# Performance work log

Hardware: AMD Instinct MI355X
Metric: run time of the kernel (lower is better)

The kernel has to match this reference:

```python
import jax, jax.numpy as jnp
import numpy as np

MAX_FEATURES = 5000
EMBED_DIM = 100
H1, H2, NUM_CLASSES = 64, 32, 4
BATCH, SEQ = 1024, 256


def _keras_lstm_scan(x_seq, mask_seq, W, U, b):
    """x_seq: [T,B,E], mask_seq: [T,B] bool. Keras gate order i,f,c,o.
    Masked steps carry (h, c) through unchanged (Keras mask_zero semantics).
    Returns (all hidden states [T,B,H], final hidden [B,H])."""
    B = x_seq.shape[1]
    H = U.shape[0]
    h0 = jnp.zeros((B, H), x_seq.dtype)
    c0 = jnp.zeros((B, H), x_seq.dtype)

    def step(carry, inp):
        h, c = carry
        x, m = inp
        z = x @ W + h @ U + b  # [B, 4H]
        i, f, g, o = jnp.split(z, 4, axis=-1)
        i = jax.nn.sigmoid(i)
        f = jax.nn.sigmoid(f)
        g = jnp.tanh(g)
        o = jax.nn.sigmoid(o)
        c_new = f * c + i * g
        h_new = o * jnp.tanh(c_new)
        m = m[:, None]
        h2 = jnp.where(m, h_new, h)
        c2 = jnp.where(m, c_new, c)
        return (h2, c2), h2

    (hT, _), hs = jax.lax.scan(step, (h0, c0), (x_seq, mask_seq))
    return hs, hT


def setup_inputs() -> dict:
    key = jax.random.key(0)
    ks = jax.random.split(key, 8)
    s = 0.05
    tokens = jax.random.randint(ks[0], (BATCH, SEQ), 0, MAX_FEATURES, dtype=jnp.int32)
    emb = jax.random.normal(ks[1], (MAX_FEATURES, EMBED_DIM), jnp.float32) * s
    W1 = jax.random.normal(ks[2], (EMBED_DIM, 4 * H1), jnp.float32) * s
    U1 = jax.random.normal(ks[3], (H1, 4 * H1), jnp.float32) * s
    b1 = jnp.zeros((4 * H1,), jnp.float32)
    W2 = jax.random.normal(ks[4], (H1, 4 * H2), jnp.float32) * s
    U2 = jax.random.normal(ks[5], (H2, 4 * H2), jnp.float32) * s
    b2 = jnp.zeros((4 * H2,), jnp.float32)
    Wd = jax.random.normal(ks[6], (H2, NUM_CLASSES), jnp.float32) * s
    bd = jnp.zeros((NUM_CLASSES,), jnp.float32)
    return {"tokens": tokens, "emb": emb, "W1": W1, "U1": U1, "b1": b1,
            "W2": W2, "U2": U2, "b2": b2, "Wd": Wd, "bd": bd}


def reference(tokens, emb, W1, U1, b1, W2, U2, b2, Wd, bd):
    mask = (tokens != 0)                       # [B,T] mask_zero=True
    x = emb[tokens]                            # [B,T,E]
    x_t = jnp.transpose(x, (1, 0, 2))          # [T,B,E]
    m_t = jnp.transpose(mask, (1, 0))          # [T,B]
    hs1, _ = _keras_lstm_scan(x_t, m_t, W1, U1, b1)   # [T,B,64]
    _, h2 = _keras_lstm_scan(hs1, m_t, W2, U2, b2)    # [B,32] last valid state
    return jax.nn.sigmoid(h2 @ Wd + bd)        # [B,4]
```

## Files before the change

### kernel.cpp

```cpp
#include <hip/hip_runtime.h>

typedef _Float16 hp2 __attribute__((ext_vector_type(2)));

#define NB    1024
#define TT    256
#define EE    100
#define VOCAB 5000
#define GG1   256
#define GG2   128

__device__ __forceinline__ float fast_sigmoid(float x) {
  return __builtin_amdgcn_rcpf(1.0f + __expf(-x));
}
__device__ __forceinline__ float fast_tanh(float x) {
  return 1.0f - 2.0f * __builtin_amdgcn_rcpf(1.0f + __expf(2.0f * x));
}

__global__ __launch_bounds__(256) void emb_gemm(
    const float* __restrict__ emb, const float* __restrict__ W1,
    const float* __restrict__ b1, float* __restrict__ emb_zi)
{
  __shared__ float sE[8][EE];
  const int j  = threadIdx.x;
  const int v0 = blockIdx.x * 8;
  for (int idx = j; idx < 8 * EE; idx += 256) {
    int r = idx / EE, k = idx % EE;
    sE[r][k] = emb[(size_t)(v0 + r) * EE + k];
  }
  __syncthreads();
  float acc[8];
  const float bb = b1[j];
  #pragma unroll
  for (int r = 0; r < 8; ++r) acc[r] = bb;
  for (int k = 0; k < EE; ++k) {
    float w = W1[k * GG1 + j];
    #pragma unroll
    for (int r = 0; r < 8; ++r) acc[r] = fmaf(sE[r][k], w, acc[r]);
  }
  const int slot = (j & 63) * 4 + (j >> 6);
  #pragma unroll
  for (int r = 0; r < 8; ++r) emb_zi[(size_t)(v0 + r) * GG1 + slot] = acc[r];
}

__global__ __launch_bounds__(64) __attribute__((amdgpu_waves_per_eu(1, 1)))
void lstm_row(
    const int* __restrict__ tokens, const float* __restrict__ emb_zi,
    const float* __restrict__ U1,
    const float* __restrict__ W2, const float* __restrict__ U2, const float* __restrict__ b2,
    const float* __restrict__ Wd, const float* __restrict__ bd,
    float* __restrict__ out)
{
  __shared__ __align__(16) _Float16 sH[96];
  __shared__ int sTok[TT];

  const int u   = threadIdx.x;
  const int row = blockIdx.x;
  const int u2  = u & 31;
  const int s   = u >> 5;

  hp2 wA[128];
  #pragma unroll
  for (int p = 0; p < 32; ++p) {
    #pragma unroll
    for (int g = 0; g < 4; ++g) {
      hp2 w;
      w[0] = (_Float16)U1[(2 * p + 0) * GG1 + g * 64 + u];
      w[1] = (_Float16)U1[(2 * p + 1) * GG1 + g * 64 + u];
      wA[4 * p + g] = w;
    }
  }
  hp2 wB[96];
  #pragma unroll
  for (int p = 0; p < 24; ++p) {
    int k0 = 48 * s + 2 * p;
    const float* r0 = (k0     < 64) ? &W2[(size_t)k0 * GG2]       : &U2[(size_t)(k0 - 64) * GG2];
    const float* r1 = (k0 + 1 < 64) ? &W2[(size_t)(k0 + 1) * GG2] : &U2[(size_t)(k0 + 1 - 64) * GG2];
    #pragma unroll
    for (int g = 0; g < 4; ++g) {
      hp2 w;
      w[0] = (_Float16)r0[g * 32 + u2];
      w[1] = (_Float16)r1[g * 32 + u2];
      wB[4 * p + g] = w;
    }
  }
  const float bi2 = b2[u2], bf2 = b2[32 + u2], bg2 = b2[64 + u2], bo2 = b2[96 + u2];

  ((int4*)sTok)[u] = ((const int4*)(tokens + (size_t)row * TT))[u];
  sH[u] = (_Float16)0.0f;
  if (u < 32) sH[64 + u] = (_Float16)0.0f;
  __syncthreads();

  float c1 = 0.f, h1 = 0.f, c2 = 0.f, h2v = 0.f;
  int tok_cur = sTok[0];
  float4 zx = *(const float4*)&emb_zi[(size_t)tok_cur * GG1 + 4 * u];

  for (int t = 0; t < TT; ++t) {
    const bool m = (tok_cur != 0);
    int tok_next = (t + 1 < TT) ? sTok[t + 1] : 0;

    float a0 = zx.x, a1 = zx.y, a2 = zx.z, a3 = zx.w;
    #pragma unroll
    for (int q = 0; q < 8; ++q) {
      int4 hq = ((const int4*)sH)[q];
      #pragma unroll
      for (int pp = 0; pp < 4; ++pp) {
        hp2 hv = ((const hp2*)&hq)[pp];
        const int p = 4 * q + pp;
        a0 = __builtin_amdgcn_fdot2(hv, wA[4 * p + 0], a0, false);
        a1 = __builtin_amdgcn_fdot2(hv, wA[4 * p + 1], a1, false);
        a2 = __builtin_amdgcn_fdot2(hv, wA[4 * p + 2], a2, false);
        a3 = __builtin_amdgcn_fdot2(hv, wA[4 * p + 3], a3, false);
      }
    }
    float4 zxn = zx;
    if (t + 1 < TT) zxn = *(const float4*)&emb_zi[(size_t)tok_next * GG1 + 4 * u];

    {
      float iv = fast_sigmoid(a0);
      float fv = fast_sigmoid(a1);
      float gv = fast_tanh(a2);
      float ov = fast_sigmoid(a3);
      if (m) { c1 = fv * c1 + iv * gv; h1 = ov * fast_tanh(c1); }
    }
    sH[u] = (_Float16)h1;
    __syncthreads();

    float b0 = 0.f, b1v = 0.f, b2v = 0.f, b3 = 0.f;
    #pragma unroll
    for (int q = 0; q < 6; ++q) {
      int4 hq = ((const int4*)sH)[6 * s + q];
      #pragma unroll
      for (int pp = 0; pp < 4; ++pp) {
        hp2 hv = ((const hp2*)&hq)[pp];
        const int p = 4 * q + pp;
        b0  = __builtin_amdgcn_fdot2(hv, wB[4 * p + 0], b0,  false);
        b1v = __builtin_amdgcn_fdot2(hv, wB[4 * p + 1], b1v, false);
        b2v = __builtin_amdgcn_fdot2(hv, wB[4 * p + 2], b2v, false);
        b3  = __builtin_amdgcn_fdot2(hv, wB[4 * p + 3], b3,  false);
      }
    }
    b0  += __shfl_xor(b0, 32);
    b1v += __shfl_xor(b1v, 32);
    b2v += __shfl_xor(b2v, 32);
    b3  += __shfl_xor(b3, 32);
    {
      float i2 = fast_sigmoid(b0 + bi2);
      float f2 = fast_sigmoid(b1v + bf2);
      float g2 = fast_tanh(b2v + bg2);
      float o2 = fast_sigmoid(b3 + bo2);
      if (m) { c2 = f2 * c2 + i2 * g2; h2v = o2 * fast_tanh(c2); }
    }
    if (s == 0) sH[64 + u2] = (_Float16)h2v;
    __syncthreads();

    tok_cur = tok_next;
    zx = zxn;
  }

  if (u < 4) {
    float a = bd[u];
    #pragma unroll
    for (int k = 0; k < 32; ++k)
      a = fmaf((float)sH[64 + k], Wd[k * 4 + u], a);
    out[(size_t)row * 4 + u] = fast_sigmoid(a);
  }
}

extern "C" void kernel_launch(void* const* d_in, const int* in_sizes, int n_in,
                              void* d_out, int out_size, void* d_ws, size_t ws_size,
                              hipStream_t stream) {
  const int*   tokens = (const int*)d_in[0];
  const float* emb    = (const float*)d_in[1];
  const float* W1     = (const float*)d_in[2];
  const float* U1     = (const float*)d_in[3];
  const float* b1     = (const float*)d_in[4];
  const float* W2     = (const float*)d_in[5];
  const float* U2     = (const float*)d_in[6];
  const float* b2     = (const float*)d_in[7];
  const float* Wd     = (const float*)d_in[8];
  const float* bd     = (const float*)d_in[9];
  float* out    = (float*)d_out;
  float* emb_zi = (float*)d_ws;

  emb_gemm<<<dim3(VOCAB / 8), dim3(256), 0, stream>>>(emb, W1, b1, emb_zi);
  lstm_row<<<dim3(NB), dim3(64), 0, stream>>>(
      tokens, emb_zi, U1, W2, U2, b2, Wd, bd, out);
}
```

Measured before the change: 241.6 us.

## Skew LSTM layers by one step with double-buffered hidden state

Layer 2 at step t now runs in the same loop iteration as layer 1 at step t+1. Both read one shared-memory buffer and write the other, which cuts the per-step barriers from two to one and lets the two layers' dot-product chains interleave for more ILP. The embedding projection prefetch moves two steps ahead, and the first layer-1 step is peeled before the loop. The cost is extra prologue code, a second small LDS buffer and a fiddlier mask and token bookkeeping, with the final layer-2 state read from buffer 0.

```diff
diff --git a/kernel.cpp b/kernel.cpp
--- a/kernel.cpp
+++ b/kernel.cpp
@@ -50,7 +50,7 @@
     const float* __restrict__ Wd, const float* __restrict__ bd,
     float* __restrict__ out)
 {
-  __shared__ __align__(16) _Float16 sH[96];
+  __shared__ __align__(16) _Float16 sHB[2][96];
   __shared__ int sTok[TT];
 
   const int u   = threadIdx.x;
@@ -86,22 +86,43 @@
   const float bi2 = b2[u2], bf2 = b2[32 + u2], bg2 = b2[64 + u2], bo2 = b2[96 + u2];
 
   ((int4*)sTok)[u] = ((const int4*)(tokens + (size_t)row * TT))[u];
-  sH[u] = (_Float16)0.0f;
-  if (u < 32) sH[64 + u] = (_Float16)0.0f;
+  sHB[0][u] = (_Float16)0.0f;
+  sHB[1][u] = (_Float16)0.0f;
+  if (u < 32) { sHB[0][64 + u] = (_Float16)0.0f; sHB[1][64 + u] = (_Float16)0.0f; }
   __syncthreads();
 
-  float c1 = 0.f, h1 = 0.f, c2 = 0.f, h2v = 0.f;
-  int tok_cur = sTok[0];
-  float4 zx = *(const float4*)&emb_zi[(size_t)tok_cur * GG1 + 4 * u];
+  float c1 = 0.f, h1r = 0.f, c2 = 0.f, h2r = 0.f;
+
+  int tok_b = sTok[0];
+  {
+    float4 zx0 = *(const float4*)&emb_zi[(size_t)tok_b * GG1 + 4 * u];
+    if (tok_b != 0) {
+      float iv = fast_sigmoid(zx0.x), fv = fast_sigmoid(zx0.y);
+      float gv = fast_tanh(zx0.z),    ov = fast_sigmoid(zx0.w);
+      (void)fv;
+      c1 = iv * gv; h1r = ov * fast_tanh(c1);
+    }
+    sHB[0][u] = (_Float16)h1r;
+  }
+  int   tok_a = sTok[1];
+  float4 zxa = *(const float4*)&emb_zi[(size_t)tok_a * GG1 + 4 * u];
+  __syncthreads();
 
   for (int t = 0; t < TT; ++t) {
-    const bool m = (tok_cur != 0);
-    int tok_next = (t + 1 < TT) ? sTok[t + 1] : 0;
-
-    float a0 = zx.x, a1 = zx.y, a2 = zx.z, a3 = zx.w;
+    const _Float16* rb = sHB[t & 1];
+    _Float16*       wb = (_Float16*)sHB[(t & 1) ^ 1];
+
+    int tok_n = 0;
+    float4 zxn = zxa;
+    if (t + 2 < TT) {
+      tok_n = sTok[t + 2];
+      zxn = *(const float4*)&emb_zi[(size_t)tok_n * GG1 + 4 * u];
+    }
+
+    float a0 = zxa.x, a1 = zxa.y, a2 = zxa.z, a3 = zxa.w;
     #pragma unroll
     for (int q = 0; q < 8; ++q) {
-      int4 hq = ((const int4*)sH)[q];
+      int4 hq = ((const int4*)rb)[q];
       #pragma unroll
       for (int pp = 0; pp < 4; ++pp) {
         hp2 hv = ((const hp2*)&hq)[pp];
@@ -112,23 +133,12 @@
         a3 = __builtin_amdgcn_fdot2(hv, wA[4 * p + 3], a3, false);
       }
     }
-    float4 zxn = zx;
-    if (t + 1 < TT) zxn = *(const float4*)&emb_zi[(size_t)tok_next * GG1 + 4 * u];
-
-    {
-      float iv = fast_sigmoid(a0);
-      float fv = fast_sigmoid(a1);
-      float gv = fast_tanh(a2);
-      float ov = fast_sigmoid(a3);
-      if (m) { c1 = fv * c1 + iv * gv; h1 = ov * fast_tanh(c1); }
-    }
-    sH[u] = (_Float16)h1;
-    __syncthreads();
 
     float b0 = 0.f, b1v = 0.f, b2v = 0.f, b3 = 0.f;
+    const int4* hbp = (const int4*)(rb + 48 * s);
     #pragma unroll
     for (int q = 0; q < 6; ++q) {
-      int4 hq = ((const int4*)sH)[6 * s + q];
+      int4 hq = hbp[q];
       #pragma unroll
       for (int pp = 0; pp < 4; ++pp) {
         hp2 hv = ((const hp2*)&hq)[pp];
@@ -139,29 +149,40 @@
         b3  = __builtin_amdgcn_fdot2(hv, wB[4 * p + 3], b3,  false);
       }
     }
+
     b0  += __shfl_xor(b0, 32);
     b1v += __shfl_xor(b1v, 32);
     b2v += __shfl_xor(b2v, 32);
     b3  += __shfl_xor(b3, 32);
     {
+      const bool mb = (tok_b != 0);
       float i2 = fast_sigmoid(b0 + bi2);
       float f2 = fast_sigmoid(b1v + bf2);
       float g2 = fast_tanh(b2v + bg2);
       float o2 = fast_sigmoid(b3 + bo2);
-      if (m) { c2 = f2 * c2 + i2 * g2; h2v = o2 * fast_tanh(c2); }
-    }
-    if (s == 0) sH[64 + u2] = (_Float16)h2v;
+      if (mb) { c2 = f2 * c2 + i2 * g2; h2r = o2 * fast_tanh(c2); }
+    }
+    if (s == 0) wb[64 + u2] = (_Float16)h2r;
+
+    {
+      const bool ma = (tok_a != 0);
+      float iv = fast_sigmoid(a0);
+      float fv = fast_sigmoid(a1);
+      float gv = fast_tanh(a2);
+      float ov = fast_sigmoid(a3);
+      if (ma) { c1 = fv * c1 + iv * gv; h1r = ov * fast_tanh(c1); }
+    }
+    wb[u] = (_Float16)h1r;
     __syncthreads();
 
-    tok_cur = tok_next;
-    zx = zxn;
+    tok_b = tok_a; tok_a = tok_n; zxa = zxn;
   }
 
   if (u < 4) {
     float a = bd[u];
     #pragma unroll
     for (int k = 0; k < 32; ++k)
-      a = fmaf((float)sH[64 + k], Wd[k * 4 + u], a);
+      a = fmaf((float)sHB[0][64 + k], Wd[k * 4 + u], a);
     out[(size_t)row * 4 + u] = fast_sigmoid(a);
   }
 }
```

Result: slower. 251.8 us (+4.2%).

## Process two batch rows per wavefront to interleave independent LSTM recurrences

Applied to the files above, without the earlier changes.

Each 64-thread block now advances two sequences at once, sharing the register-resident U1/W2/U2 weights and issuing two independent dot-product chains per step. The aim is to hide the latency of the serial recurrence and barriers with a second independent stream of work, and to halve the per-block weight loading. In exchange the grid is halved to 512 blocks, which on a 256-CU part may leave fewer waves per CU, and each thread needs more registers.

```diff
diff --git a/kernel.cpp b/kernel.cpp
--- a/kernel.cpp
+++ b/kernel.cpp
@@ -43,18 +43,18 @@
 }
 
 __global__ __launch_bounds__(64) __attribute__((amdgpu_waves_per_eu(1, 1)))
-void lstm_row(
+void lstm_row2(
     const int* __restrict__ tokens, const float* __restrict__ emb_zi,
     const float* __restrict__ U1,
     const float* __restrict__ W2, const float* __restrict__ U2, const float* __restrict__ b2,
     const float* __restrict__ Wd, const float* __restrict__ bd,
     float* __restrict__ out)
 {
-  __shared__ __align__(16) _Float16 sH[96];
-  __shared__ int sTok[TT];
+  __shared__ __align__(16) _Float16 sH[2][96];
+  __shared__ int sTok[2][TT];
 
   const int u   = threadIdx.x;
-  const int row = blockIdx.x;
+  const int b   = blockIdx.x;
   const int u2  = u & 31;
   const int s   = u >> 5;
 
@@ -85,84 +85,114 @@
   }
   const float bi2 = b2[u2], bf2 = b2[32 + u2], bg2 = b2[64 + u2], bo2 = b2[96 + u2];
 
-  ((int4*)sTok)[u] = ((const int4*)(tokens + (size_t)row * TT))[u];
-  sH[u] = (_Float16)0.0f;
-  if (u < 32) sH[64 + u] = (_Float16)0.0f;
+  ((int4*)sTok[0])[u] = ((const int4*)(tokens + (size_t)(2 * b + 0) * TT))[u];
+  ((int4*)sTok[1])[u] = ((const int4*)(tokens + (size_t)(2 * b + 1) * TT))[u];
+  sH[0][u] = (_Float16)0.0f;
+  sH[1][u] = (_Float16)0.0f;
+  if (u < 32) { sH[0][64 + u] = (_Float16)0.0f; sH[1][64 + u] = (_Float16)0.0f; }
   __syncthreads();
 
-  float c1 = 0.f, h1 = 0.f, c2 = 0.f, h2v = 0.f;
-  int tok_cur = sTok[0];
-  float4 zx = *(const float4*)&emb_zi[(size_t)tok_cur * GG1 + 4 * u];
+  float c1A = 0.f, h1A = 0.f, c2A = 0.f, h2A = 0.f;
+  float c1B = 0.f, h1B = 0.f, c2B = 0.f, h2B = 0.f;
+  int tokA = sTok[0][0];
+  int tokB = sTok[1][0];
+  float4 zxA = *(const float4*)&emb_zi[(size_t)tokA * GG1 + 4 * u];
+  float4 zxB = *(const float4*)&emb_zi[(size_t)tokB * GG1 + 4 * u];
 
   for (int t = 0; t < TT; ++t) {
-    const bool m = (tok_cur != 0);
-    int tok_next = (t + 1 < TT) ? sTok[t + 1] : 0;
-
-    float a0 = zx.x, a1 = zx.y, a2 = zx.z, a3 = zx.w;
+    const bool mA = (tokA != 0), mB = (tokB != 0);
+    int tokAn = 0, tokBn = 0;
+    if (t + 1 < TT) { tokAn = sTok[0][t + 1]; tokBn = sTok[1][t + 1]; }
+
+    float aA0 = zxA.x, aA1 = zxA.y, aA2 = zxA.z, aA3 = zxA.w;
+    float aB0 = zxB.x, aB1 = zxB.y, aB2 = zxB.z, aB3 = zxB.w;
     #pragma unroll
     for (int q = 0; q < 8; ++q) {
-      int4 hq = ((const int4*)sH)[q];
+      int4 hqA = ((const int4*)sH[0])[q];
+      int4 hqB = ((const int4*)sH[1])[q];
       #pragma unroll
       for (int pp = 0; pp < 4; ++pp) {
-        hp2 hv = ((const hp2*)&hq)[pp];
         const int p = 4 * q + pp;
-        a0 = __builtin_amdgcn_fdot2(hv, wA[4 * p + 0], a0, false);
-        a1 = __builtin_amdgcn_fdot2(hv, wA[4 * p + 1], a1, false);
-        a2 = __builtin_amdgcn_fdot2(hv, wA[4 * p + 2], a2, false);
-        a3 = __builtin_amdgcn_fdot2(hv, wA[4 * p + 3], a3, false);
+        hp2 hvA = ((const hp2*)&hqA)[pp];
+        hp2 hvB = ((const hp2*)&hqB)[pp];
+        aA0 = __builtin_amdgcn_fdot2(hvA, wA[4 * p + 0], aA0, false);
+        aA1 = __builtin_amdgcn_fdot2(hvA, wA[4 * p + 1], aA1, false);
+        aA2 = __builtin_amdgcn_fdot2(hvA, wA[4 * p + 2], aA2, false);
+        aA3 = __builtin_amdgcn_fdot2(hvA, wA[4 * p + 3], aA3, false);
+        aB0 = __builtin_amdgcn_fdot2(hvB, wA[4 * p + 0], aB0, false);
+        aB1 = __builtin_amdgcn_fdot2(hvB, wA[4 * p + 1], aB1, false);
+        aB2 = __builtin_amdgcn_fdot2(hvB, wA[4 * p + 2], aB2, false);
+        aB3 = __builtin_amdgcn_fdot2(hvB, wA[4 * p + 3], aB3, false);
       }
     }
-    float4 zxn = zx;
-    if (t + 1 < TT) zxn = *(const float4*)&emb_zi[(size_t)tok_next * GG1 + 4 * u];
-
+    float4 zxAn = zxA, zxBn = zxB;
+    if (t + 1 < TT) {
+      zxAn = *(const float4*)&emb_zi[(size_t)tokAn * GG1 + 4 * u];
+      zxBn = *(const float4*)&emb_zi[(size_t)tokBn * GG1 + 4 * u];
+    }
     {
-      float iv = fast_sigmoid(a0);
-      float fv = fast_sigmoid(a1);
-      float gv = fast_tanh(a2);
-      float ov = fast_sigmoid(a3);
-      if (m) { c1 = fv * c1 + iv * gv; h1 = ov * fast_tanh(c1); }
-    }
-    sH[u] = (_Float16)h1;
+      float iv = fast_sigmoid(aA0), fv = fast_sigmoid(aA1);
+      float gv = fast_tanh(aA2),    ov = fast_sigmoid(aA3);
+      if (mA) { c1A = fv * c1A + iv * gv; h1A = ov * fast_tanh(c1A); }
+      float iw = fast_sigmoid(aB0), fw = fast_sigmoid(aB1);
+      float gw = fast_tanh(aB2),    ow = fast_sigmoid(aB3);
+      if (mB) { c1B = fw * c1B + iw * gw; h1B = ow * fast_tanh(c1B); }
+    }
+    sH[0][u] = (_Float16)h1A;
+    sH[1][u] = (_Float16)h1B;
     __syncthreads();
 
-    float b0 = 0.f, b1v = 0.f, b2v = 0.f, b3 = 0.f;
+    float bA0 = 0.f, bA1 = 0.f, bA2 = 0.f, bA3 = 0.f;
+    float bB0 = 0.f, bB1 = 0.f, bB2 = 0.f, bB3 = 0.f;
+    const int4* hpA = (const int4*)(&sH[0][48 * s]);
+    const int4* hpB = (const int4*)(&sH[1][48 * s]);
     #pragma unroll
     for (int q = 0; q < 6; ++q) {
-      int4 hq = ((const int4*)sH)[6 * s + q];
+      int4 hqA = hpA[q];
+      int4 hqB = hpB[q];
       #pragma unroll
       for (int pp = 0; pp < 4; ++pp) {
-        hp2 hv = ((const hp2*)&hq)[pp];
         const int p = 4 * q + pp;
-        b0  = __builtin_amdgcn_fdot2(hv, wB[4 * p + 0], b0,  false);
-        b1v = __builtin_amdgcn_fdot2(hv, wB[4 * p + 1], b1v, false);
-        b2v = __builtin_amdgcn_fdot2(hv, wB[4 * p + 2], b2v, false);
-        b3  = __builtin_amdgcn_fdot2(hv, wB[4 * p + 3], b3,  false);
+        hp2 hvA = ((const hp2*)&hqA)[pp];
+        hp2 hvB = ((const hp2*)&hqB)[pp];
+        bA0 = __builtin_amdgcn_fdot2(hvA, wB[4 * p + 0], bA0, false);
+        bA1 = __builtin_amdgcn_fdot2(hvA, wB[4 * p + 1], bA1, false);
+        bA2 = __builtin_amdgcn_fdot2(hvA, wB[4 * p + 2], bA2, false);
+        bA3 = __builtin_amdgcn_fdot2(hvA, wB[4 * p + 3], bA3, false);
+        bB0 = __builtin_amdgcn_fdot2(hvB, wB[4 * p + 0], bB0, false);
+        bB1 = __builtin_amdgcn_fdot2(hvB, wB[4 * p + 1], bB1, false);
+        bB2 = __builtin_amdgcn_fdot2(hvB, wB[4 * p + 2], bB2, false);
+        bB3 = __builtin_amdgcn_fdot2(hvB, wB[4 * p + 3], bB3, false);
       }
     }
-    b0  += __shfl_xor(b0, 32);
-    b1v += __shfl_xor(b1v, 32);
-    b2v += __shfl_xor(b2v, 32);
-    b3  += __shfl_xor(b3, 32);
+    bA0 += __shfl_xor(bA0, 32); bA1 += __shfl_xor(bA1, 32);
+    bA2 += __shfl_xor(bA2, 32); bA3 += __shfl_xor(bA3, 32);
+    bB0 += __shfl_xor(bB0, 32); bB1 += __shfl_xor(bB1, 32);
+    bB2 += __shfl_xor(bB2, 32); bB3 += __shfl_xor(bB3, 32);
     {
-      float i2 = fast_sigmoid(b0 + bi2);
-      float f2 = fast_sigmoid(b1v + bf2);
-      float g2 = fast_tanh(b2v + bg2);
-      float o2 = fast_sigmoid(b3 + bo2);
-      if (m) { c2 = f2 * c2 + i2 * g2; h2v = o2 * fast_tanh(c2); }
-    }
-    if (s == 0) sH[64 + u2] = (_Float16)h2v;
+      float i2 = fast_sigmoid(bA0 + bi2), f2 = fast_sigmoid(bA1 + bf2);
+      float g2 = fast_tanh(bA2 + bg2),    o2 = fast_sigmoid(bA3 + bo2);
+      if (mA) { c2A = f2 * c2A + i2 * g2; h2A = o2 * fast_tanh(c2A); }
+      float i3 = fast_sigmoid(bB0 + bi2), f3 = fast_sigmoid(bB1 + bf2);
+      float g3 = fast_tanh(bB2 + bg2),    o3 = fast_sigmoid(bB3 + bo2);
+      if (mB) { c2B = f3 * c2B + i3 * g3; h2B = o3 * fast_tanh(c2B); }
+    }
+    if (s == 0) {
+      sH[0][64 + u2] = (_Float16)h2A;
+      sH[1][64 + u2] = (_Float16)h2B;
+    }
     __syncthreads();
 
-    tok_cur = tok_next;
-    zx = zxn;
-  }
-
-  if (u < 4) {
-    float a = bd[u];
+    tokA = tokAn; tokB = tokBn; zxA = zxAn; zxB = zxBn;
+  }
+
+  if (u < 8) {
+    int r = u >> 2, o = u & 3;
+    float a = bd[o];
     #pragma unroll
     for (int k = 0; k < 32; ++k)
-      a = fmaf((float)sH[64 + k], Wd[k * 4 + u], a);
-    out[(size_t)row * 4 + u] = fast_sigmoid(a);
+      a = fmaf((float)sH[r][64 + k], Wd[k * 4 + o], a);
+    out[(size_t)(2 * b + r) * 4 + o] = fast_sigmoid(a);
   }
 }
 
@@ -183,6 +213,6 @@
   float* emb_zi = (float*)d_ws;
 
   emb_gemm<<<dim3(VOCAB / 8), dim3(256), 0, stream>>>(emb, W1, b1, emb_zi);
-  lstm_row<<<dim3(NB), dim3(64), 0, stream>>>(
+  lstm_row2<<<dim3(NB / 2), dim3(64), 0, stream>>>(
       tokens, emb_zi, U1, W2, U2, b2, Wd, bd, out);
 }
```

Result: slower. 487.4 us (+101.7%).

## Batch 16 rows per block with MFMA recurrences and layer-pipelined waves

Applied to the files above, without the earlier changes.

Replaces the one-row-per-64-thread-block LSTM with blocks that each process 16 batch rows and compute both recurrent matmuls with 16x16x16 fp16 MFMA instructions. Four waves compute layer 1 and two waves compute layer 2. Layer 2 runs one timestep behind layer 1 through a double-buffered shared fragment buffer, so each timestep needs a single barrier. This targets the serial dot-product latency and the low occupancy of the old per-row scheme. The costs are only 64 blocks for the whole batch, a larger per-step critical path through a 6-wave barrier, and fragment-layout indexing that is easy to get wrong.

```diff
diff --git a/kernel.cpp b/kernel.cpp
--- a/kernel.cpp
+++ b/kernel.cpp
@@ -1,6 +1,7 @@
 #include <hip/hip_runtime.h>
 
-typedef _Float16 hp2 __attribute__((ext_vector_type(2)));
+typedef _Float16 h4 __attribute__((ext_vector_type(4)));
+typedef float    f4v __attribute__((ext_vector_type(4)));
 
 #define NB    1024
 #define TT    256
@@ -8,6 +9,8 @@
 #define VOCAB 5000
 #define GG1   256
 #define GG2   128
+#define RPB   16
+#define NTHR  384
 
 __device__ __forceinline__ float fast_sigmoid(float x) {
   return __builtin_amdgcn_rcpf(1.0f + __expf(-x));
@@ -42,127 +45,179 @@
   for (int r = 0; r < 8; ++r) emb_zi[(size_t)(v0 + r) * GG1 + slot] = acc[r];
 }
 
-__global__ __launch_bounds__(64) __attribute__((amdgpu_waves_per_eu(1, 1)))
-void lstm_row(
+__global__ __launch_bounds__(NTHR, 2) void lstm_mfma(
     const int* __restrict__ tokens, const float* __restrict__ emb_zi,
     const float* __restrict__ U1,
     const float* __restrict__ W2, const float* __restrict__ U2, const float* __restrict__ b2,
     const float* __restrict__ Wd, const float* __restrict__ bd,
     float* __restrict__ out)
 {
-  __shared__ __align__(16) _Float16 sH[96];
-  __shared__ int sTok[TT];
-
-  const int u   = threadIdx.x;
-  const int row = blockIdx.x;
-  const int u2  = u & 31;
-  const int s   = u >> 5;
-
-  hp2 wA[128];
-  #pragma unroll
-  for (int p = 0; p < 32; ++p) {
-    #pragma unroll
-    for (int g = 0; g < 4; ++g) {
-      hp2 w;
-      w[0] = (_Float16)U1[(2 * p + 0) * GG1 + g * 64 + u];
-      w[1] = (_Float16)U1[(2 * p + 1) * GG1 + g * 64 + u];
-      wA[4 * p + g] = w;
+  __shared__ __align__(16) _Float16 fbuf[2][6][256];
+  __shared__ __align__(16) int sTokT[TT][16];
+  __shared__ float hfin[RPB][32];
+
+  const int tid  = threadIdx.x;
+  const int w    = tid >> 6;
+  const int l    = tid & 63;
+  const int lr   = l & 15;
+  const int lg   = l >> 4;
+  const int row0 = blockIdx.x * RPB;
+
+  h4 wB[4][6];
+  float bias2[4] = {0.f, 0.f, 0.f, 0.f};
+  if (w < 4) {
+    #pragma unroll
+    for (int gi = 0; gi < 4; ++gi) {
+      #pragma unroll
+      for (int c = 0; c < 4; ++c) {
+        h4 v;
+        #pragma unroll
+        for (int jj = 0; jj < 4; ++jj) {
+          int k = 16 * c + lg * 4 + jj;
+          v[jj] = (_Float16)U1[k * GG1 + 64 * gi + 16 * w + lr];
+        }
+        wB[gi][c] = v;
+      }
     }
-  }
-  hp2 wB[96];
-  #pragma unroll
-  for (int p = 0; p < 24; ++p) {
-    int k0 = 48 * s + 2 * p;
-    const float* r0 = (k0     < 64) ? &W2[(size_t)k0 * GG2]       : &U2[(size_t)(k0 - 64) * GG2];
-    const float* r1 = (k0 + 1 < 64) ? &W2[(size_t)(k0 + 1) * GG2] : &U2[(size_t)(k0 + 1 - 64) * GG2];
-    #pragma unroll
-    for (int g = 0; g < 4; ++g) {
-      hp2 w;
-      w[0] = (_Float16)r0[g * 32 + u2];
-      w[1] = (_Float16)r1[g * 32 + u2];
-      wB[4 * p + g] = w;
+  } else {
+    const int w2 = w - 4;
+    #pragma unroll
+    for (int gi = 0; gi < 4; ++gi) {
+      #pragma unroll
+      for (int c = 0; c < 6; ++c) {
+        h4 v;
+        #pragma unroll
+        for (int jj = 0; jj < 4; ++jj) {
+          int k  = 16 * c + lg * 4 + jj;
+          int j2 = 32 * gi + 16 * w2 + lr;
+          float x = (k < 64) ? W2[k * GG2 + j2] : U2[(k - 64) * GG2 + j2];
+          v[jj] = (_Float16)x;
+        }
+        wB[gi][c] = v;
+      }
+      bias2[gi] = b2[32 * gi + 16 * w2 + lr];
     }
   }
-  const float bi2 = b2[u2], bf2 = b2[32 + u2], bg2 = b2[64 + u2], bo2 = b2[96 + u2];
-
-  ((int4*)sTok)[u] = ((const int4*)(tokens + (size_t)row * TT))[u];
-  sH[u] = (_Float16)0.0f;
-  if (u < 32) sH[64 + u] = (_Float16)0.0f;
+
+  for (int idx = tid; idx < RPB * TT; idx += NTHR) {
+    int m = idx >> 8, t = idx & 255;
+    sTokT[t][m] = tokens[(size_t)(row0 + m) * TT + t];
+  }
+  for (int idx = tid; idx < 2 * 6 * 256; idx += NTHR)
+    ((_Float16*)fbuf)[idx] = (_Float16)0.0f;
   __syncthreads();
 
-  float c1 = 0.f, h1 = 0.f, c2 = 0.f, h2v = 0.f;
-  int tok_cur = sTok[0];
-  float4 zx = *(const float4*)&emb_zi[(size_t)tok_cur * GG1 + 4 * u];
-
-  for (int t = 0; t < TT; ++t) {
-    const bool m = (tok_cur != 0);
-    int tok_next = (t + 1 < TT) ? sTok[t + 1] : 0;
-
-    float a0 = zx.x, a1 = zx.y, a2 = zx.z, a3 = zx.w;
-    #pragma unroll
-    for (int q = 0; q < 8; ++q) {
-      int4 hq = ((const int4*)sH)[q];
-      #pragma unroll
-      for (int pp = 0; pp < 4; ++pp) {
-        hp2 hv = ((const hp2*)&hq)[pp];
-        const int p = 4 * q + pp;
-        a0 = __builtin_amdgcn_fdot2(hv, wA[4 * p + 0], a0, false);
-        a1 = __builtin_amdgcn_fdot2(hv, wA[4 * p + 1], a1, false);
-        a2 = __builtin_amdgcn_fdot2(hv, wA[4 * p + 2], a2, false);
-        a3 = __builtin_amdgcn_fdot2(hv, wA[4 * p + 3], a3, false);
+  float c1v[4] = {0.f,0.f,0.f,0.f}, h1v[4] = {0.f,0.f,0.f,0.f};
+  float c2v[4] = {0.f,0.f,0.f,0.f}, h2v[4] = {0.f,0.f,0.f,0.f};
+
+  f4v zx[4];
+  if (w < 4) {
+    int4 tk0 = *(const int4*)&sTokT[0][lg * 4];
+    const int uu = 16 * w + lr;
+    zx[0] = *(const f4v*)&emb_zi[(size_t)tk0.x * GG1 + uu * 4];
+    zx[1] = *(const f4v*)&emb_zi[(size_t)tk0.y * GG1 + uu * 4];
+    zx[2] = *(const f4v*)&emb_zi[(size_t)tk0.z * GG1 + uu * 4];
+    zx[3] = *(const f4v*)&emb_zi[(size_t)tk0.w * GG1 + uu * 4];
+  }
+
+  for (int t = 0; t <= TT; ++t) {
+    const int p = t & 1;
+    if (w < 4) {
+      if (t < TT) {
+        h4 a0 = *(const h4*)&fbuf[p][0][l * 4];
+        h4 a1 = *(const h4*)&fbuf[p][1][l * 4];
+        h4 a2 = *(const h4*)&fbuf[p][2][l * 4];
+        h4 a3 = *(const h4*)&fbuf[p][3][l * 4];
+        f4v ac[4];
+        #pragma unroll
+        for (int gi = 0; gi < 4; ++gi) {
+          f4v s;
+          s[0] = zx[0][gi]; s[1] = zx[1][gi]; s[2] = zx[2][gi]; s[3] = zx[3][gi];
+          s = __builtin_amdgcn_mfma_f32_16x16x16f16(a0, wB[gi][0], s, 0, 0, 0);
+          s = __builtin_amdgcn_mfma_f32_16x16x16f16(a1, wB[gi][1], s, 0, 0, 0);
+          s = __builtin_amdgcn_mfma_f32_16x16x16f16(a2, wB[gi][2], s, 0, 0, 0);
+          s = __builtin_amdgcn_mfma_f32_16x16x16f16(a3, wB[gi][3], s, 0, 0, 0);
+          ac[gi] = s;
+        }
+        f4v zn[4];
+        #pragma unroll
+        for (int i = 0; i < 4; ++i) zn[i] = zx[i];
+        if (t + 1 < TT) {
+          int4 tkn = *(const int4*)&sTokT[t + 1][lg * 4];
+          const int uu = 16 * w + lr;
+          zn[0] = *(const f4v*)&emb_zi[(size_t)tkn.x * GG1 + uu * 4];
+          zn[1] = *(const f4v*)&emb_zi[(size_t)tkn.y * GG1 + uu * 4];
+          zn[2] = *(const f4v*)&emb_zi[(size_t)tkn.z * GG1 + uu * 4];
+          zn[3] = *(const f4v*)&emb_zi[(size_t)tkn.w * GG1 + uu * 4];
+        }
+        int4 tk = *(const int4*)&sTokT[t][lg * 4];
+        int tka[4] = {tk.x, tk.y, tk.z, tk.w};
+        #pragma unroll
+        for (int i = 0; i < 4; ++i) {
+          float iv = fast_sigmoid(ac[0][i]);
+          float fv = fast_sigmoid(ac[1][i]);
+          float gv = fast_tanh(ac[2][i]);
+          float ov = fast_sigmoid(ac[3][i]);
+          float cn = fv * c1v[i] + iv * gv;
+          if (tka[i] != 0) { c1v[i] = cn; h1v[i] = ov * fast_tanh(cn); }
+          fbuf[p ^ 1][w][(lg * 4 + i + 16 * (lr >> 2)) * 4 + (lr & 3)] = (_Float16)h1v[i];
+        }
+        #pragma unroll
+        for (int i = 0; i < 4; ++i) zx[i] = zn[i];
+      }
+    } else {
+      if (t >= 1) {
+        const int tt = t - 1;
+        const int w2 = w - 4;
+        h4 a0 = *(const h4*)&fbuf[p][0][l * 4];
+        h4 a1 = *(const h4*)&fbuf[p][1][l * 4];
+        h4 a2 = *(const h4*)&fbuf[p][2][l * 4];
+        h4 a3 = *(const h4*)&fbuf[p][3][l * 4];
+        h4 a4 = *(const h4*)&fbuf[p][4][l * 4];
+        h4 a5 = *(const h4*)&fbuf[p][5][l * 4];
+        f4v ac[4];
+        #pragma unroll
+        for (int gi = 0; gi < 4; ++gi) {
+          f4v s;
+          s[0] = bias2[gi]; s[1] = bias2[gi]; s[2] = bias2[gi]; s[3] = bias2[gi];
+          s = __builtin_amdgcn_mfma_f32_16x16x16f16(a0, wB[gi][0], s, 0, 0, 0);
+          s = __builtin_amdgcn_mfma_f32_16x16x16f16(a1, wB[gi][1], s, 0, 0, 0);
+          s = __builtin_amdgcn_mfma_f32_16x16x16f16(a2, wB[gi][2], s, 0, 0, 0);
+          s = __builtin_amdgcn_mfma_f32_16x16x16f16(a3, wB[gi][3], s, 0, 0, 0);
+          s = __builtin_amdgcn_mfma_f32_16x16x16f16(a4, wB[gi][4], s, 0, 0, 0);
+          s = __builtin_amdgcn_mfma_f32_16x16x16f16(a5, wB[gi][5], s, 0, 0, 0);
+          ac[gi] = s;
+        }
+        int4 tk = *(const int4*)&sTokT[tt][lg * 4];
+        int tka[4] = {tk.x, tk.y, tk.z, tk.w};
+        #pragma unroll
+        for (int i = 0; i < 4; ++i) {
+          float iv = fast_sigmoid(ac[0][i]);
+          float fv = fast_sigmoid(ac[1][i]);
+          float gv = fast_tanh(ac[2][i]);
+          float ov = fast_sigmoid(ac[3][i]);
+          float cn = fv * c2v[i] + iv * gv;
+          if (tka[i] != 0) { c2v[i] = cn; h2v[i] = ov * fast_tanh(cn); }
+          fbuf[p ^ 1][4 + w2][(lg * 4 + i + 16 * (lr >> 2)) * 4 + (lr & 3)] = (_Float16)h2v[i];
+        }
       }
     }
-    float4 zxn = zx;
-    if (t + 1 < TT) zxn = *(const float4*)&emb_zi[(size_t)tok_next * GG1 + 4 * u];
-
-    {
-      float iv = fast_sigmoid(a0);
-      float fv = fast_sigmoid(a1);
-      float gv = fast_tanh(a2);
-      float ov = fast_sigmoid(a3);
-      if (m) { c1 = fv * c1 + iv * gv; h1 = ov * fast_tanh(c1); }
-    }
-    sH[u] = (_Float16)h1;
     __syncthreads();
-
-    float b0 = 0.f, b1v = 0.f, b2v = 0.f, b3 = 0.f;
-    #pragma unroll
-    for (int q = 0; q < 6; ++q) {
-      int4 hq = ((const int4*)sH)[6 * s + q];
-      #pragma unroll
-      for (int pp = 0; pp < 4; ++pp) {
-        hp2 hv = ((const hp2*)&hq)[pp];
-        const int p = 4 * q + pp;
-        b0  = __builtin_amdgcn_fdot2(hv, wB[4 * p + 0], b0,  false);
-        b1v = __builtin_amdgcn_fdot2(hv, wB[4 * p + 1], b1v, false);
-        b2v = __builtin_amdgcn_fdot2(hv, wB[4 * p + 2], b2v, false);
-        b3  = __builtin_amdgcn_fdot2(hv, wB[4 * p + 3], b3,  false);
-      }
-    }
-    b0  += __shfl_xor(b0, 32);
-    b1v += __shfl_xor(b1v, 32);
-    b2v += __shfl_xor(b2v, 32);
-    b3  += __shfl_xor(b3, 32);
-    {
-      float i2 = fast_sigmoid(b0 + bi2);
-      float f2 = fast_sigmoid(b1v + bf2);
-      float g2 = fast_tanh(b2v + bg2);
-      float o2 = fast_sigmoid(b3 + bo2);
-      if (m) { c2 = f2 * c2 + i2 * g2; h2v = o2 * fast_tanh(c2); }
-    }
-    if (s == 0) sH[64 + u2] = (_Float16)h2v;
-    __syncthreads();
-
-    tok_cur = tok_next;
-    zx = zxn;
-  }
-
-  if (u < 4) {
-    float a = bd[u];
+  }
+
+  if (w >= 4) {
+    const int w2 = w - 4, u2 = 16 * w2 + lr;
+    #pragma unroll
+    for (int i = 0; i < 4; ++i) hfin[lg * 4 + i][u2] = h2v[i];
+  }
+  __syncthreads();
+  if (tid < 64) {
+    int m = tid >> 2, o = tid & 3;
+    float a = bd[o];
     #pragma unroll
     for (int k = 0; k < 32; ++k)
-      a = fmaf((float)sH[64 + k], Wd[k * 4 + u], a);
-    out[(size_t)row * 4 + u] = fast_sigmoid(a);
+      a = fmaf(hfin[m][k], Wd[k * 4 + o], a);
+    out[(size_t)(row0 + m) * 4 + o] = fast_sigmoid(a);
   }
 }
 
@@ -183,6 +238,6 @@
   float* emb_zi = (float*)d_ws;
 
   emb_gemm<<<dim3(VOCAB / 8), dim3(256), 0, stream>>>(emb, W1, b1, emb_zi);
-  lstm_row<<<dim3(NB), dim3(64), 0, stream>>>(
+  lstm_mfma<<<dim3(NB / RPB), dim3(NTHR), 0, stream>>>(
       tokens, emb_zi, U1, W2, U2, b2, Wd, bd, out);
 }
```

Result: slower. 284.3 us (+17.7%).
